# Optimization experiments

Hardware: AMD Instinct MI355X
Metric: run time of the kernel (lower is better)

Reference implementation:

```python
import jax, jax.numpy as jnp
import numpy as np

B, C, H, W = 16, 512, 32, 32
NH, HD = 8, 64
CTX_DIM, L = 768, 512
EPS = 1e-5


def setup_inputs() -> dict:
    key = jax.random.key(0)
    ks = jax.random.split(key, 10)
    x = jax.random.normal(ks[0], (B, C, H, W), dtype=jnp.float32)
    context = jax.random.normal(ks[1], (B, L, CTX_DIM), dtype=jnp.float32)
    context_mask = jax.random.randint(ks[2], (B, L), 0, 2).astype(bool)
    context_mask = context_mask.at[:, 0].set(True)  # guarantee >=1 valid key per row
    s = 0.02
    ln_w = jnp.ones((C,), jnp.float32)
    ln_b = jnp.zeros((C,), jnp.float32)
    Wq = jax.random.normal(ks[3], (C, C), jnp.float32) * s
    Wk = jax.random.normal(ks[4], (C, C), jnp.float32) * s
    Wv = jax.random.normal(ks[5], (C, C), jnp.float32) * s
    Wo = jax.random.normal(ks[6], (C, C), jnp.float32) * s
    Wctx = jax.random.normal(ks[7], (C, CTX_DIM), jnp.float32) * s
    return {"x": x, "context": context, "context_mask": context_mask,
            "ln_w": ln_w, "ln_b": ln_b, "Wq": Wq, "Wk": Wk, "Wv": Wv,
            "Wo": Wo, "Wctx": Wctx}


def _layernorm(x, w, b):
    mu = jnp.mean(x, axis=-1, keepdims=True)
    var = jnp.mean(jnp.square(x - mu), axis=-1, keepdims=True)
    return (x - mu) * jax.lax.rsqrt(var + EPS) * w + b


def reference(x, context, context_mask, ln_w, ln_b, Wq, Wk, Wv, Wo, Wctx):
    b, c, h, w = x.shape
    n = h * w
    hidden = x.reshape(b, c, n).transpose(0, 2, 1)          # [b, n, c]
    hidden_norm = _layernorm(hidden, ln_w, ln_b)
    ctx = jnp.einsum('bld,cd->blc', context, Wctx)          # context_proj

    q = jnp.einsum('bnc,ec->bne', hidden_norm, Wq).reshape(b, n, NH, HD).transpose(0, 2, 1, 3)
    k = jnp.einsum('blc,ec->ble', ctx, Wk).reshape(b, -1, NH, HD).transpose(0, 2, 1, 3)
    v = jnp.einsum('blc,ec->ble', ctx, Wv).reshape(b, -1, NH, HD).transpose(0, 2, 1, 3)

    scale = HD ** -0.5
    scores = jnp.einsum('bhnd,bhld->bhnl', q, k) * scale    # [b,H,n,L]
    mask4 = context_mask[:, None, None, :]                  # [b,1,1,L]
    scores = jnp.where(mask4, scores, -jnp.inf)
    all_invalid = ~jnp.any(mask4, axis=-1, keepdims=True)   # [b,1,1,1]
    scores = jnp.where(all_invalid, 0.0, scores)
    attn = jax.nn.softmax(scores, axis=-1)
    attn = jnp.where(mask4, attn, 0.0)
    attn = jnp.where(all_invalid, 0.0, attn)

    out = jnp.einsum('bhnl,bhld->bhnd', attn, v)            # [b,H,n,hd]
    out = out.transpose(0, 2, 1, 3).reshape(b, n, c)
    out = jnp.einsum('bnc,ec->bne', out, Wo)
    out = out + hidden
    return out.transpose(0, 2, 1).reshape(b, c, h, w)
```

## Files before the change

kernel.cpp:

```cpp
#include <hip/hip_runtime.h>

#define B_   16
#define C_   512
#define N_   1024
#define L_   512
#define CTX_ 768
#define NH_  8
#define HD_  64
#define EPS_ 1e-5f

typedef short bfrag __attribute__((ext_vector_type(8)));
typedef float f32x4 __attribute__((ext_vector_type(4)));

__device__ __forceinline__ ushort f2bf(float f) {
  union { float f; unsigned u; } v; v.f = f;
  unsigned r = v.u + 0x7fffu + ((v.u >> 16) & 1u);
  return (ushort)(r >> 16);
}

__device__ __forceinline__ f32x4 mfma16(bfrag a, bfrag b, f32x4 c) {
  return __builtin_amdgcn_mfma_f32_16x16x32_bf16(a, b, c, 0, 0, 0);
}

__device__ __forceinline__ void g2l16(const ushort* g, ushort* l) {
  __builtin_amdgcn_global_load_lds(
      (const __attribute__((address_space(1))) void*)g,
      (__attribute__((address_space(3))) void*)l, 16, 0, 0);
}

__global__ __launch_bounds__(256) void cast5_kernel(
    const float* __restrict__ s0, const float* __restrict__ s1,
    const float* __restrict__ s2, const float* __restrict__ s3,
    const float* __restrict__ s4,
    ushort* __restrict__ d0, ushort* __restrict__ d1, ushort* __restrict__ d2,
    ushort* __restrict__ d3, ushort* __restrict__ d4) {
  int i = blockIdx.x * 256 + threadIdx.x;
  const float* src; ushort* dst; int off;
  if      (i < 98304)  { src = s0; dst = d0; off = i; }
  else if (i < 163840) { src = s1; dst = d1; off = i - 98304; }
  else if (i < 229376) { src = s2; dst = d2; off = i - 163840; }
  else if (i < 294912) { src = s3; dst = d3; off = i - 229376; }
  else                 { src = s4; dst = d4; off = i - 294912; }
  float4 vv = ((const float4*)src)[off];
  ushort4 o;
  o.x = f2bf(vv.x); o.y = f2bf(vv.y); o.z = f2bf(vv.z); o.w = f2bf(vv.w);
  ((ushort4*)dst)[off] = o;
}

__global__ __launch_bounds__(1024) void ln_kernel(const float* __restrict__ x,
                                                  const float* __restrict__ w,
                                                  const float* __restrict__ bia,
                                                  ushort* __restrict__ hn) {
  const int b  = blockIdx.x;
  const int n0 = blockIdx.y * 64;
  const int tid = threadIdx.x;
  const int nx = tid & 63, cg = tid >> 6;
  const float* xb = x + (size_t)b * C_ * N_;

  float s = 0.f, s2 = 0.f;
  for (int c = cg; c < C_; c += 16) {
    float v = xb[(size_t)c * N_ + n0 + nx];
    s += v; s2 += v * v;
  }
  __shared__ float red[2][16][64];
  __shared__ float mean[64], rstd[64];
  red[0][cg][nx] = s; red[1][cg][nx] = s2;
  __syncthreads();
  if (cg == 0) {
    float ss = 0.f, ss2 = 0.f;
#pragma unroll
    for (int i = 0; i < 16; ++i) { ss += red[0][i][nx]; ss2 += red[1][i][nx]; }
    float mu  = ss * (1.f / C_);
    float var = ss2 * (1.f / C_) - mu * mu;
    mean[nx] = mu;
    rstd[nx] = rsqrtf(var + EPS_);
  }
  __syncthreads();

  __shared__ float tile[64][65];
  for (int ct = 0; ct < 8; ++ct) {
    const int c0 = ct * 64;
    for (int cy = cg; cy < 64; cy += 16)
      tile[cy][nx] = xb[(size_t)(c0 + cy) * N_ + n0 + nx];
    __syncthreads();
    const int cx = tid & 63, ng = tid >> 6;
    const float wv = w[c0 + cx], bv = bia[c0 + cx];
    for (int ny = ng; ny < 64; ny += 16) {
      float val = (tile[cx][ny] - mean[ny]) * rstd[ny] * wv + bv;
      hn[((size_t)b * N_ + n0 + ny) * C_ + c0 + cx] = f2bf(val);
    }
    __syncthreads();
  }
}

__device__ __forceinline__ void gemm_core(const ushort* __restrict__ A,
                                          const ushort* __restrict__ W,
                                          int K, ushort* la, ushort* lb,
                                          f32x4 acc[4][4],
                                          int tid, int wm, int we, int col, int rg) {
  const int lane = tid & 63, w = tid >> 6;
  const int rloc = lane >> 2, pt = lane & 3;
  const int pts = pt ^ ((rloc >> 1) & 3);
  const int qsel = (rg ^ ((col >> 1) & 3)) * 8;

  for (int k0 = 0; k0 < K; k0 += 32) {
#pragma unroll
    for (int c = 0; c < 2; ++c) {
      const int chunk = w + c * 4;
      const int row = chunk * 16 + rloc;
      g2l16(A + (size_t)row * K + k0 + pts * 8, la + chunk * 512);
      g2l16(W + (size_t)row * K + k0 + pts * 8, lb + chunk * 512);
    }
    __syncthreads();
    bfrag af[4], bf[4];
#pragma unroll
    for (int i = 0; i < 4; ++i) {
      af[i] = *(const bfrag*)&la[(wm + i * 16 + col) * 32 + qsel];
      bf[i] = *(const bfrag*)&lb[(we + i * 16 + col) * 32 + qsel];
    }
#pragma unroll
    for (int i = 0; i < 4; ++i)
#pragma unroll
      for (int j = 0; j < 4; ++j)
        acc[i][j] = mfma16(af[i], bf[j], acc[i][j]);
    __syncthreads();
  }
}

__global__ __launch_bounds__(256) void gemm_g(const ushort* __restrict__ A,
                                              const ushort* __restrict__ W,
                                              ushort* __restrict__ out, int K) {
  __shared__ ushort la[128 * 32];
  __shared__ ushort lb[128 * 32];
  const int m0 = blockIdx.x * 128, e0 = blockIdx.y * 128;
  const int tid = threadIdx.x, lane = tid & 63, w = tid >> 6;
  const int wm = (w >> 1) * 64, we = (w & 1) * 64;
  const int col = lane & 15, rg = lane >> 4;

  f32x4 acc[4][4] = {};
  gemm_core(A + (size_t)m0 * K, W + (size_t)e0 * K, K, la, lb, acc, tid, wm, we, col, rg);

#pragma unroll
  for (int i = 0; i < 4; ++i)
#pragma unroll
    for (int j = 0; j < 4; ++j)
#pragma unroll
      for (int r = 0; r < 4; ++r)
        out[(size_t)(m0 + wm + i * 16 + rg * 4 + r) * 512 + e0 + we + j * 16 + col] =
            f2bf(acc[i][j][r]);
}

__global__ __launch_bounds__(256) void gemm_kv(const ushort* __restrict__ A,
                                               const ushort* __restrict__ Wk,
                                               const ushort* __restrict__ Wv,
                                               ushort* __restrict__ Ko,
                                               ushort* __restrict__ Vo) {
  __shared__ ushort la[128 * 32];
  __shared__ ushort lb[128 * 32];
  const int isv = blockIdx.y >> 2;
  const ushort* W = isv ? Wv : Wk;
  ushort* out = isv ? Vo : Ko;
  const int m0 = blockIdx.x * 128, e0 = (blockIdx.y & 3) * 128;
  const int tid = threadIdx.x, lane = tid & 63, w = tid >> 6;
  const int wm = (w >> 1) * 64, we = (w & 1) * 64;
  const int col = lane & 15, rg = lane >> 4;

  f32x4 acc[4][4] = {};
  gemm_core(A + (size_t)m0 * C_, W + (size_t)e0 * C_, C_, la, lb, acc, tid, wm, we, col, rg);

#pragma unroll
  for (int i = 0; i < 4; ++i)
#pragma unroll
    for (int j = 0; j < 4; ++j)
#pragma unroll
      for (int r = 0; r < 4; ++r)
        out[(size_t)(m0 + wm + i * 16 + rg * 4 + r) * 512 + e0 + we + j * 16 + col] =
            f2bf(acc[i][j][r]);
}

__global__ __launch_bounds__(256) void gemm_res(const ushort* __restrict__ A,
                                                const ushort* __restrict__ W,
                                                const float* __restrict__ x,
                                                float* __restrict__ out) {
  __shared__ ushort la[128 * 32];
  __shared__ ushort lb[128 * 32];
  __shared__ float T[16][132];
  const int m0 = blockIdx.x * 128, e0 = blockIdx.y * 128;
  const int tid = threadIdx.x, lane = tid & 63, w = tid >> 6;
  const int wm = (w >> 1) * 64, we = (w & 1) * 64;
  const int col = lane & 15, rg = lane >> 4;

  f32x4 acc[4][4] = {};
  gemm_core(A + (size_t)m0 * C_, W + (size_t)e0 * C_, C_, la, lb, acc, tid, wm, we, col, rg);

  const int b = m0 >> 10, n0l = m0 & 1023;
#pragma unroll
  for (int g = 0; g < 8; ++g) {
    if ((w & 1) == (g >> 2)) {
      const int j = g & 3;
#pragma unroll
      for (int i = 0; i < 4; ++i)
        *(f32x4*)&T[col][wm + i * 16 + rg * 4] = acc[i][j];
    }
    __syncthreads();
    const int n = tid & 127;
    for (int cc = tid >> 7; cc < 16; cc += 2) {
      const int c = e0 + g * 16 + cc;
      const size_t idx = (size_t)b * C_ * N_ + (size_t)c * N_ + n0l + n;
      out[idx] = T[cc][n] + x[idx];
    }
    __syncthreads();
  }
}

__global__ __launch_bounds__(256) void gemm_ctx(const float* __restrict__ Ap,
                                                const ushort* __restrict__ W,
                                                ushort* __restrict__ outp) {
  __shared__ ushort la[128 * 40];
  __shared__ ushort lb[128 * 40];
  const int m0 = blockIdx.x * 128, e0 = blockIdx.y * 128;
  const int tid = threadIdx.x, lane = tid & 63, w = tid >> 6;
  const int wm = (w >> 1) * 64, we = (w & 1) * 64;
  const int col = lane & 15, rg = lane >> 4;
  const int srow = tid >> 1, sh = (tid & 1) * 16;
  const int K = CTX_;

  f32x4 acc[4][4] = {};

  for (int k0 = 0; k0 < K; k0 += 32) {
    {
      const float* ap = &Ap[(size_t)(m0 + srow) * K + k0 + sh];
      float4 f0 = ((const float4*)ap)[0];
      float4 f1 = ((const float4*)ap)[1];
      float4 f2 = ((const float4*)ap)[2];
      float4 f3 = ((const float4*)ap)[3];
      union { int4 v; ushort u[8]; } p0, p1;
      p0.u[0] = f2bf(f0.x); p0.u[1] = f2bf(f0.y); p0.u[2] = f2bf(f0.z); p0.u[3] = f2bf(f0.w);
      p0.u[4] = f2bf(f1.x); p0.u[5] = f2bf(f1.y); p0.u[6] = f2bf(f1.z); p0.u[7] = f2bf(f1.w);
      p1.u[0] = f2bf(f2.x); p1.u[1] = f2bf(f2.y); p1.u[2] = f2bf(f2.z); p1.u[3] = f2bf(f2.w);
      p1.u[4] = f2bf(f3.x); p1.u[5] = f2bf(f3.y); p1.u[6] = f2bf(f3.z); p1.u[7] = f2bf(f3.w);
      *(int4*)&la[srow * 40 + sh]     = p0.v;
      *(int4*)&la[srow * 40 + sh + 8] = p1.v;
      const ushort* wp = &W[(size_t)(e0 + srow) * K + k0 + sh];
      *(int4*)&lb[srow * 40 + sh]     = *(const int4*)wp;
      *(int4*)&lb[srow * 40 + sh + 8] = *(const int4*)(wp + 8);
    }
    __syncthreads();
    bfrag af[4], bf[4];
#pragma unroll
    for (int i = 0; i < 4; ++i) {
      af[i] = *(const bfrag*)&la[(wm + i * 16 + col) * 40 + rg * 8];
      bf[i] = *(const bfrag*)&lb[(we + i * 16 + col) * 40 + rg * 8];
    }
#pragma unroll
    for (int i = 0; i < 4; ++i)
#pragma unroll
      for (int j = 0; j < 4; ++j)
        acc[i][j] = mfma16(af[i], bf[j], acc[i][j]);
    __syncthreads();
  }

#pragma unroll
  for (int i = 0; i < 4; ++i)
#pragma unroll
    for (int j = 0; j < 4; ++j)
#pragma unroll
      for (int r = 0; r < 4; ++r)
        outp[(size_t)(m0 + wm + i * 16 + rg * 4 + r) * 512 + e0 + we + j * 16 + col] =
            f2bf(acc[i][j][r]);
}

__global__ __launch_bounds__(256) void attn_mfma(const ushort* __restrict__ q,
                                                 const ushort* __restrict__ k,
                                                 const ushort* __restrict__ v,
                                                 const int* __restrict__ mask,
                                                 ushort* __restrict__ o) {
  __shared__ ushort Kl[64 * 72];
  __shared__ ushort Vt[64 * 72];
  __shared__ ushort Pw[4][32 * 76];
  __shared__ float mlb[64];

  const int h = blockIdx.y, b = blockIdx.z;
  const int q0 = blockIdx.x * 128;
  const int tid = threadIdx.x, lane = tid & 63, w = tid >> 6;
  const int col = lane & 15, rg = lane >> 4;
  const int wq = w * 32;
  const float C1 = 0.18033688011112042f;

  bfrag qf[2][2];
#pragma unroll
  for (int mi = 0; mi < 2; ++mi)
#pragma unroll
    for (int kc = 0; kc < 2; ++kc)
      qf[mi][kc] = *(const bfrag*)
          &q[((size_t)b * N_ + q0 + wq + mi * 16 + col) * C_ + h * HD_ + kc * 32 + rg * 8];

  f32x4 oa[2][4] = {};
  float l_part[2][4] = {};

  for (int l0 = 0; l0 < L_; l0 += 64) {
#pragma unroll
    for (int it = 0; it < 2; ++it) {
      const int idx = it * 256 + tid;
      const int key = idx >> 3, part = idx & 7;
      *(int4*)&Kl[key * 72 + part * 8] =
          *(const int4*)&k[((size_t)b * L_ + l0 + key) * C_ + h * HD_ + part * 8];
    }
#pragma unroll
    for (int it = 0; it < 4; ++it) {
      const int idx = it * 256 + tid;
      const int key = idx & 63, d0 = (idx >> 6) * 4;
      ushort4 vv = *(const ushort4*)&v[((size_t)b * L_ + l0 + key) * C_ + h * HD_ + d0];
      Vt[(d0 + 0) * 72 + key] = vv.x;
      Vt[(d0 + 1) * 72 + key] = vv.y;
      Vt[(d0 + 2) * 72 + key] = vv.z;
      Vt[(d0 + 3) * 72 + key] = vv.w;
    }
    if (tid < 64) mlb[tid] = mask[b * L_ + l0 + tid] ? 0.f : -1e30f;
    __syncthreads();

    f32x4 s[2][4] = {};
#pragma unroll
    for (int kc = 0; kc < 2; ++kc) {
      bfrag kf[4];
#pragma unroll
      for (int ni = 0; ni < 4; ++ni)
        kf[ni] = *(const bfrag*)&Kl[(ni * 16 + col) * 72 + kc * 32 + rg * 8];
#pragma unroll
      for (int mi = 0; mi < 2; ++mi)
#pragma unroll
        for (int ni = 0; ni < 4; ++ni)
          s[mi][ni] = mfma16(qf[mi][kc], kf[ni], s[mi][ni]);
    }
#pragma unroll
    for (int ni = 0; ni < 4; ++ni) {
      const float bias = mlb[ni * 16 + col];
#pragma unroll
      for (int mi = 0; mi < 2; ++mi)
#pragma unroll
        for (int r = 0; r < 4; ++r) {
          const float p = exp2f(fmaf(s[mi][ni][r], C1, bias));
          s[mi][ni][r] = p;
          l_part[mi][r] += p;
        }
    }
#pragma unroll
    for (int mi = 0; mi < 2; ++mi)
#pragma unroll
      for (int ni = 0; ni < 4; ++ni)
#pragma unroll
        for (int r = 0; r < 4; ++r)
          Pw[w][(mi * 16 + rg * 4 + r) * 76 + ni * 16 + col] = f2bf(s[mi][ni][r]);
#pragma unroll
    for (int kc = 0; kc < 2; ++kc) {
      bfrag pf[2], vf[4];
#pragma unroll
      for (int mi = 0; mi < 2; ++mi)
        pf[mi] = *(const bfrag*)&Pw[w][(mi * 16 + col) * 76 + kc * 32 + rg * 8];
#pragma unroll
      for (int di = 0; di < 4; ++di)
        vf[di] = *(const bfrag*)&Vt[(di * 16 + col) * 72 + kc * 32 + rg * 8];
#pragma unroll
      for (int mi = 0; mi < 2; ++mi)
#pragma unroll
        for (int di = 0; di < 4; ++di)
          oa[mi][di] = mfma16(pf[mi], vf[di], oa[mi][di]);
    }
    __syncthreads();
  }

#pragma unroll
  for (int mi = 0; mi < 2; ++mi) {
#pragma unroll
    for (int r = 0; r < 4; ++r) {
      float l = l_part[mi][r];
      l += __shfl_xor(l, 1);
      l += __shfl_xor(l, 2);
      l += __shfl_xor(l, 4);
      l += __shfl_xor(l, 8);
      const float inv = 1.f / l;
      const size_t row = (size_t)b * N_ + q0 + wq + mi * 16 + rg * 4 + r;
#pragma unroll
      for (int di = 0; di < 4; ++di)
        o[row * C_ + h * HD_ + di * 16 + col] = f2bf(oa[mi][di][r] * inv);
    }
  }
}

extern "C" void kernel_launch(void* const* d_in, const int* in_sizes, int n_in,
                              void* d_out, int out_size, void* d_ws, size_t ws_size,
                              hipStream_t stream) {
  (void)in_sizes; (void)n_in; (void)out_size; (void)ws_size;
  const float* x       = (const float*)d_in[0];
  const float* context = (const float*)d_in[1];
  const int*   mask    = (const int*)d_in[2];
  const float* ln_w    = (const float*)d_in[3];
  const float* ln_b    = (const float*)d_in[4];
  const float* Wq      = (const float*)d_in[5];
  const float* Wk      = (const float*)d_in[6];
  const float* Wv      = (const float*)d_in[7];
  const float* Wo      = (const float*)d_in[8];
  const float* Wctx    = (const float*)d_in[9];

  char* wsb = (char*)d_ws;
  ushort* qb    = (ushort*)(wsb + 0);
  ushort* kb    = (ushort*)(wsb + 16777216);
  ushort* vb    = (ushort*)(wsb + 25165824);
  ushort* hn    = (ushort*)(wsb + 33554432);
  ushort* ctx   = (ushort*)(wsb + 50331648);
  ushort* wctxb = (ushort*)(wsb + 58720256);
  ushort* wqb   = (ushort*)(wsb + 59506688);
  ushort* wkb   = (ushort*)(wsb + 60030976);
  ushort* wvb   = (ushort*)(wsb + 60555264);
  ushort* wob   = (ushort*)(wsb + 61079552);

  cast5_kernel<<<1408, 256, 0, stream>>>(Wctx, Wq, Wk, Wv, Wo,
                                         wctxb, wqb, wkb, wvb, wob);
  ln_kernel<<<dim3(B_, N_ / 64), 1024, 0, stream>>>(x, ln_w, ln_b, hn);
  gemm_ctx<<<dim3(64, 4), 256, 0, stream>>>(context, wctxb, ctx);
  gemm_kv<<<dim3(64, 8), 256, 0, stream>>>(ctx, wkb, wvb, kb, vb);
  gemm_g<<<dim3(128, 4), 256, 0, stream>>>(hn, wqb, qb, C_);
  attn_mfma<<<dim3(N_ / 128, NH_, B_), 256, 0, stream>>>(qb, kb, vb, mask, hn);
  gemm_res<<<dim3(128, 4), 256, 0, stream>>>(hn, wob, x, (float*)d_out);
}
```

Measured before the change: 180.8 us.

## Keep attention probabilities in registers via transposed QK^T and K16 MFMA

Computes S^T by swapping MFMA operands so each lane holds four consecutive keys for one query. These can then be packed straight into bf16 A-fragments for a 16x16x16 MFMA against V, which removes the per-warp LDS round trip for P (store, read-back and the Pw buffer). It also uses packed bf16 conversion and reduces row sums with cross-lane shuffles plus bpermute. The cost is twice as many smaller-K MFMAs for the PV product and narrower V fragment loads from LDS.

New measurement: 174.4 us. 1.04x faster.

```diff
diff --git a/kernel.cpp b/kernel.cpp
--- a/kernel.cpp
+++ b/kernel.cpp
@@ -9,8 +9,9 @@
 #define HD_  64
 #define EPS_ 1e-5f
 
-typedef short bfrag __attribute__((ext_vector_type(8)));
-typedef float f32x4 __attribute__((ext_vector_type(4)));
+typedef short bfrag  __attribute__((ext_vector_type(8)));
+typedef short bfrag4 __attribute__((ext_vector_type(4)));
+typedef float f32x4  __attribute__((ext_vector_type(4)));
 
 __device__ __forceinline__ ushort f2bf(float f) {
   union { float f; unsigned u; } v; v.f = f;
@@ -20,6 +21,14 @@
 
 __device__ __forceinline__ f32x4 mfma16(bfrag a, bfrag b, f32x4 c) {
   return __builtin_amdgcn_mfma_f32_16x16x32_bf16(a, b, c, 0, 0, 0);
+}
+__device__ __forceinline__ f32x4 mfma16k16(bfrag4 a, bfrag4 b, f32x4 c) {
+  return __builtin_amdgcn_mfma_f32_16x16x16bf16_1k(a, b, c, 0, 0, 0);
+}
+__device__ __forceinline__ unsigned cvt_pk_bf16(float lo, float hi) {
+  unsigned d;
+  asm("v_cvt_pk_bf16_f32 %0, %1, %2" : "=v"(d) : "v"(lo), "v"(hi));
+  return d;
 }
 
 __device__ __forceinline__ void g2l16(const ushort* g, ushort* l) {
@@ -277,7 +286,6 @@
                                                  ushort* __restrict__ o) {
   __shared__ ushort Kl[64 * 72];
   __shared__ ushort Vt[64 * 72];
-  __shared__ ushort Pw[4][32 * 76];
   __shared__ float mlb[64];
 
   const int h = blockIdx.y, b = blockIdx.z;
@@ -296,7 +304,7 @@
           &q[((size_t)b * N_ + q0 + wq + mi * 16 + col) * C_ + h * HD_ + kc * 32 + rg * 8];
 
   f32x4 oa[2][4] = {};
-  float l_part[2][4] = {};
+  float l_part[2] = {0.f, 0.f};
 
   for (int l0 = 0; l0 < L_; l0 += 64) {
 #pragma unroll
@@ -319,7 +327,7 @@
     if (tid < 64) mlb[tid] = mask[b * L_ + l0 + tid] ? 0.f : -1e30f;
     __syncthreads();
 
-    f32x4 s[2][4] = {};
+    f32x4 s2[2][4] = {};
 #pragma unroll
     for (int kc = 0; kc < 2; ++kc) {
       bfrag kf[4];
@@ -330,61 +338,61 @@
       for (int mi = 0; mi < 2; ++mi)
 #pragma unroll
         for (int ni = 0; ni < 4; ++ni)
-          s[mi][ni] = mfma16(qf[mi][kc], kf[ni], s[mi][ni]);
-    }
+          s2[mi][ni] = mfma16(kf[ni], qf[mi][kc], s2[mi][ni]);
+    }
+    bfrag4 pf[2][4];
 #pragma unroll
     for (int ni = 0; ni < 4; ++ni) {
-      const float bias = mlb[ni * 16 + col];
+      const f32x4 bias4 = *(const f32x4*)&mlb[ni * 16 + rg * 4];
+#pragma unroll
+      for (int mi = 0; mi < 2; ++mi) {
+        const float p0 = exp2f(fmaf(s2[mi][ni][0], C1, bias4[0]));
+        const float p1 = exp2f(fmaf(s2[mi][ni][1], C1, bias4[1]));
+        const float p2 = exp2f(fmaf(s2[mi][ni][2], C1, bias4[2]));
+        const float p3 = exp2f(fmaf(s2[mi][ni][3], C1, bias4[3]));
+        l_part[mi] += (p0 + p1) + (p2 + p3);
+        union { bfrag4 v; unsigned u[2]; } pk;
+        pk.u[0] = cvt_pk_bf16(p0, p1);
+        pk.u[1] = cvt_pk_bf16(p2, p3);
+        pf[mi][ni] = pk.v;
+      }
+    }
+#pragma unroll
+    for (int ni = 0; ni < 4; ++ni) {
+      bfrag4 vf[4];
+#pragma unroll
+      for (int di = 0; di < 4; ++di)
+        vf[di] = *(const bfrag4*)&Vt[(di * 16 + col) * 72 + ni * 16 + rg * 4];
 #pragma unroll
       for (int mi = 0; mi < 2; ++mi)
 #pragma unroll
-        for (int r = 0; r < 4; ++r) {
-          const float p = exp2f(fmaf(s[mi][ni][r], C1, bias));
-          s[mi][ni][r] = p;
-          l_part[mi][r] += p;
-        }
-    }
-#pragma unroll
-    for (int mi = 0; mi < 2; ++mi)
-#pragma unroll
-      for (int ni = 0; ni < 4; ++ni)
-#pragma unroll
-        for (int r = 0; r < 4; ++r)
-          Pw[w][(mi * 16 + rg * 4 + r) * 76 + ni * 16 + col] = f2bf(s[mi][ni][r]);
-#pragma unroll
-    for (int kc = 0; kc < 2; ++kc) {
-      bfrag pf[2], vf[4];
-#pragma unroll
-      for (int mi = 0; mi < 2; ++mi)
-        pf[mi] = *(const bfrag*)&Pw[w][(mi * 16 + col) * 76 + kc * 32 + rg * 8];
+        for (int di = 0; di < 4; ++di)
+          oa[mi][di] = mfma16k16(pf[mi][ni], vf[di], oa[mi][di]);
+    }
+    __syncthreads();
+  }
+
+  float linv[2][4];
+#pragma unroll
+  for (int mi = 0; mi < 2; ++mi) {
+    float l = l_part[mi];
+    l += __shfl_xor(l, 16);
+    l += __shfl_xor(l, 32);
+#pragma unroll
+    for (int r = 0; r < 4; ++r) {
+      int lv = __builtin_amdgcn_ds_bpermute((rg * 4 + r) * 4, __float_as_int(l));
+      linv[mi][r] = 1.f / __int_as_float(lv);
+    }
+  }
+#pragma unroll
+  for (int mi = 0; mi < 2; ++mi)
+#pragma unroll
+    for (int r = 0; r < 4; ++r) {
+      const size_t row = (size_t)b * N_ + q0 + wq + mi * 16 + rg * 4 + r;
 #pragma unroll
       for (int di = 0; di < 4; ++di)
-        vf[di] = *(const bfrag*)&Vt[(di * 16 + col) * 72 + kc * 32 + rg * 8];
-#pragma unroll
-      for (int mi = 0; mi < 2; ++mi)
-#pragma unroll
-        for (int di = 0; di < 4; ++di)
-          oa[mi][di] = mfma16(pf[mi], vf[di], oa[mi][di]);
-    }
-    __syncthreads();
-  }
-
-#pragma unroll
-  for (int mi = 0; mi < 2; ++mi) {
-#pragma unroll
-    for (int r = 0; r < 4; ++r) {
-      float l = l_part[mi][r];
-      l += __shfl_xor(l, 1);
-      l += __shfl_xor(l, 2);
-      l += __shfl_xor(l, 4);
-      l += __shfl_xor(l, 8);
-      const float inv = 1.f / l;
-      const size_t row = (size_t)b * N_ + q0 + wq + mi * 16 + rg * 4 + r;
-#pragma unroll
-      for (int di = 0; di < 4; ++di)
-        o[row * C_ + h * HD_ + di * 16 + col] = f2bf(oa[mi][di][r] * inv);
-    }
-  }
+        o[row * C_ + h * HD_ + di * 16 + col] = f2bf(oa[mi][di][r] * linv[mi][r]);
+    }
 }
 
 extern "C" void kernel_launch(void* const* d_in, const int* in_sizes, int n_in,
```
